# Performance work log

Hardware: AMD Instinct MI355X
Metric: run time of the kernel (lower is better)

## Reference

```python
import jax, jax.numpy as jnp
import numpy as np

B, D, H, W = 2, 32, 192, 192
N_SIGMA = 3
K = 8  # max instance id; ids are 1..K, 0 = background
FG_W = 1.0
W_INST, W_VAR, W_SEED = 1.0, 10.0, 1.0


def _make_xyzm():
    # channel 0 = x (varies along W), 1 = y (along H), 2 = z (along D); pixel_{x,y,z}=1
    xm = jnp.broadcast_to(jnp.linspace(0.0, 1.0, W).reshape(1, 1, W), (D, H, W))
    ym = jnp.broadcast_to(jnp.linspace(0.0, 1.0, H).reshape(1, H, 1), (D, H, W))
    zm = jnp.broadcast_to(jnp.linspace(0.0, 1.0, D).reshape(D, 1, 1), (D, H, W))
    return jnp.stack([xm, ym, zm], 0)  # (3, D, H, W)


def setup_inputs() -> dict:
    key = jax.random.key(0)
    k1, k2, k3, k4 = jax.random.split(key, 4)
    prediction = jax.random.normal(k1, (B, 3 + N_SIGMA + 1, D, H, W), jnp.float32)
    instances = jax.random.randint(k2, (B, D, H, W), 0, K + 1, jnp.int32)
    labels = jax.random.randint(k3, (B, D, H, W), 0, 2, jnp.int32)
    center_images = jax.random.uniform(k4, (B, D, H, W)) < 5e-4  # sparse center flags
    return {"prediction": prediction, "xyzm": _make_xyzm(),
            "instances": instances, "labels": labels, "center_images": center_images}


def _lovasz_hinge_flat(logits, labels):
    # logits, labels: (N,) flat; labels in {0,1} float
    signs = 2.0 * labels - 1.0
    errors = 1.0 - logits * signs
    order = jnp.argsort(-errors)          # descending errors
    errors_s = errors[order]
    gt_s = labels[order]
    gts = gt_s.sum()
    inter = gts - jnp.cumsum(gt_s)
    union = gts + jnp.cumsum(1.0 - gt_s)
    jacc = 1.0 - inter / union
    grad = jnp.concatenate([jacc[:1], jacc[1:] - jacc[:-1]])
    return jnp.dot(jax.nn.relu(errors_s), jax.lax.stop_gradient(grad))


def _forward(prediction, xyzm, instances, labels, center_images):
    def per_batch(pred, inst, lab, cim):
        emb = jnp.tanh(pred[0:3]) + xyzm                      # (3,D,H,W)
        sigma = pred[3:3 + N_SIGMA]                           # (ns,D,H,W)
        seed = jax.nn.sigmoid(pred[3 + N_SIGMA])              # (D,H,W)
        ids = jnp.arange(1, K + 1)
        masks = (inst[None] == ids[:, None, None, None]).astype(pred.dtype)  # (K,D,H,W)
        counts = masks.sum(axis=(1, 2, 3))                    # (K,)
        valid = counts > 0
        safe = jnp.maximum(counts, 1.0)
        # center: single flagged center voxel if exactly one, else masked mean of coords
        mean_center = jnp.einsum('kdhw,cdhw->kc', masks, xyzm) / safe[:, None]
        cmask = masks * cim[None].astype(pred.dtype)
        cm_cnt = cmask.sum(axis=(1, 2, 3))
        cm_center = jnp.einsum('kdhw,cdhw->kc', cmask, xyzm)
        center = jnp.where((cm_cnt == 1.0)[:, None], cm_center, mean_center)  # (K,3)
        # sigma stats per instance; var term vs detached mean, expanded form
        m_sig = jnp.einsum('kdhw,cdhw->kc', masks, sigma)
        m_sig2 = jnp.einsum('kdhw,cdhw->kc', masks, sigma * sigma)
        s_mean = m_sig / safe[:, None]                        # (K,ns)
        s_sg = jax.lax.stop_gradient(s_mean)
        var_sum = m_sig2 - 2.0 * s_sg * m_sig + s_sg * s_sg * counts[:, None]
        var_k = var_sum.sum(1) / (N_SIGMA * safe)
        s_exp = jnp.exp(10.0 * s_mean)                        # (K,ns)
        # sum_c s_c*(emb_c-center_c)^2, expanded to avoid a (K,3,D,H,W) temp
        d2 = (jnp.einsum('kc,cdhw->kdhw', s_exp, emb * emb)
              - 2.0 * jnp.einsum('kc,cdhw->kdhw', s_exp * center, emb)
              + (s_exp * center * center).sum(1)[:, None, None, None])
        dist = jnp.exp(-d2)                                   # (K,D,H,W)
        inst_k = jax.vmap(_lovasz_hinge_flat)(
            (2.0 * dist - 1.0).reshape(K, -1), masks.reshape(K, -1))
        obj = jnp.maximum(valid.sum(), 1).astype(pred.dtype)
        instance_loss = jnp.where(valid, inst_k, 0.0).sum() / obj
        var_loss = jnp.where(valid, var_k, 0.0).sum() / obj
        bg = (lab == 0).astype(pred.dtype)
        seed_loss = (bg * seed * seed).sum()
        seed_loss = seed_loss + FG_W * (masks * (seed[None] - jax.lax.stop_gradient(dist)) ** 2).sum()
        seed_loss = seed_loss / (D * H * W)
        return W_INST * instance_loss + W_VAR * var_loss + W_SEED * seed_loss

    losses = jax.vmap(per_batch)(prediction, instances, labels, center_images)
    return losses.mean()


def reference(prediction, xyzm, instances, labels, center_images):
    return _forward(prediction, xyzm, instances, labels, center_images)
```

## Files before the change

kernel.cpp:

```cpp
#include <hip/hip_runtime.h>
#include <stdint.h>

typedef unsigned long long u64;
typedef unsigned int u32;

#define BN 2
#define DD 32
#define HH 192
#define WW 192
#define NV (DD*HH*WW)
#define KK 8
#define NSL_S 576
#define VPB_S 2048
#define NSL_H 288
#define VPB_H 4096
#define NB 256
#define BOFF 1808
#define SCALE 4294967296.0f
#define L2E 1.44269504f

__device__ __forceinline__ u64 fx(float v){ return (u64)(long long)llrintf(v*SCALE); }
__device__ __forceinline__ float unfx(u64 v){ return (float)((double)(long long)v*(1.0/4294967296.0)); }
__device__ __forceinline__ float rcp_f(float x){ return __builtin_amdgcn_rcpf(x); }
__device__ __forceinline__ float exp2_f(float x){ return __builtin_amdgcn_exp2f(x); }
__device__ __forceinline__ float tanh_f(float x){ return 1.f - 2.f*rcp_f(1.f + exp2_f(x*(2.f*L2E))); }
__device__ __forceinline__ float sigm_f(float x){ return rcp_f(1.f + exp2_f(-x*L2E)); }
__device__ __forceinline__ float rfl(float x){ return __uint_as_float(__builtin_amdgcn_readfirstlane((int)__float_as_uint(x))); }

__global__ void k_detect(const u32* __restrict__ w, int nwords, u32* flags){
    u32 fF=0,fB=0,fO=0,f1=0;
    for (int i = blockIdx.x*blockDim.x + threadIdx.x; i < nwords; i += gridDim.x*blockDim.x){
        u32 x = w[i];
        if (x == 0x3F800000u) fF = 1;
        else if (x > 1u) fB = 1;
        else if (x == 1u){ f1 = 1; if (i & 1) fO = 1; }
    }
    if (fF) atomicOr(&flags[0], 1u);
    if (fB) atomicOr(&flags[1], 1u);
    if (fO) atomicOr(&flags[2], 1u);
    if (f1) atomicOr(&flags[3], 1u);
}

__global__ __launch_bounds__(512, 8) void k_stats(
        const float* __restrict__ pred,
        const int* __restrict__ inst, const int* __restrict__ lab,
        const void* __restrict__ cim, const u32* __restrict__ flags,
        u64* __restrict__ ssh, u64* __restrict__ bgsh){
    int sx = blockIdx.x, b = blockIdx.y;
    __shared__ u64 bins[8][4][KK][9];
    __shared__ u64 cmb[8][KK][4];
    __shared__ u64 bgsum;
    for (int i = threadIdx.x; i < 8*4*KK*9; i += 512) ((u64*)bins)[i] = 0ull;
    for (int i = threadIdx.x; i < 8*KK*4; i += 512) ((u64*)cmb)[i] = 0ull;
    if (threadIdx.x == 0) bgsum = 0ull;
    __syncthreads();
    int mode = flags[0] ? 2 : (flags[1] ? 1 : (flags[2] ? 0 : (flags[3] ? 3 : 0)));
    const float* pb = pred + (size_t)b*7*NV;
    const int* ib = inst + (size_t)b*NV;
    const int* lb = lab + (size_t)b*NV;
    int wv = threadIdx.x >> 6, lp = threadIdx.x & 3;
    int g = sx*VPB_S + threadIdx.x*4;

    float4 s0v = *(const float4*)&pb[3*(size_t)NV + g];
    float4 s1v = *(const float4*)&pb[4*(size_t)NV + g];
    float4 s2v = *(const float4*)&pb[5*(size_t)NV + g];
    float4 s6v = *(const float4*)&pb[6*(size_t)NV + g];
    int4 iv4 = *(const int4*)&ib[g];
    int4 lb4 = *(const int4*)&lb[g];
    int iy = g / WW;
    int ix = g - iy*WW;
    int iz = iy / HH; iy -= iz*HH;
    u64 fdx = fx(1.f/(WW-1));
    u64 fxm = fx(ix*(1.f/(WW-1)));
    u64 fym = fx(iy*(1.f/(HH-1)));
    u64 fzm = fx(iz*(1.f/(DD-1)));
    u32 cv4 = 0;
    size_t gi = (size_t)b*NV + g;
    if (mode == 0){
        int4 c = *(const int4*)&((const int*)cim)[gi];
        cv4 = (c.x?1u:0u)|(c.y?2u:0u)|(c.z?4u:0u)|(c.w?8u:0u);
    } else if (mode == 1){
        u32 c = *(const u32*)&((const unsigned char*)cim)[gi];
        cv4 = ((c&0xFFu)?1u:0u)|((c&0xFF00u)?2u:0u)|((c&0xFF0000u)?4u:0u)|((c&0xFF000000u)?8u:0u);
    } else if (mode == 2){
        float4 c = *(const float4*)&((const float*)cim)[gi];
        cv4 = (c.x!=0.f?1u:0u)|(c.y!=0.f?2u:0u)|(c.z!=0.f?4u:0u)|(c.w!=0.f?8u:0u);
    } else {
        int4 c0 = *(const int4*)&((const int*)cim)[2*gi];
        int4 c1 = *(const int4*)&((const int*)cim)[2*gi + 4];
        cv4 = (c0.x?1u:0u)|(c0.z?2u:0u)|(c1.x?4u:0u)|(c1.z?8u:0u);
    }
    float s0a[4] = {s0v.x,s0v.y,s0v.z,s0v.w};
    float s1a[4] = {s1v.x,s1v.y,s1v.z,s1v.w};
    float s2a[4] = {s2v.x,s2v.y,s2v.z,s2v.w};
    float s6a[4] = {s6v.x,s6v.y,s6v.z,s6v.w};
    int iva[4] = {iv4.x,iv4.y,iv4.z,iv4.w};
    int lba[4] = {lb4.x,lb4.y,lb4.z,lb4.w};
    float bgacc = 0.f;
    #pragma unroll
    for (int j = 0; j < 4; j++){
        float seed = sigm_f(s6a[j]);
        if (lba[j] == 0) bgacc += seed*seed;
        int iv = iva[j];
        if (iv >= 1 && iv <= KK){
            u64* bn = &bins[wv][lp][iv-1][0];
            u32 cv = (cv4 >> j) & 1u;
            atomicAdd(&bn[0], (1ull << 32) | (u64)cv);
            atomicAdd(&bn[1], fxm + (u64)j*fdx);
            atomicAdd(&bn[2], fym);
            atomicAdd(&bn[3], fzm);
            atomicAdd(&bn[4], fx(s0a[j]));
            atomicAdd(&bn[5], fx(s1a[j]));
            atomicAdd(&bn[6], fx(s2a[j]));
            atomicAdd(&bn[7], fx(s0a[j]*s0a[j] + s1a[j]*s1a[j] + s2a[j]*s2a[j]));
            if (cv){
                u64* cb = &cmb[wv][iv-1][0];
                atomicAdd(&cb[0], fxm + (u64)j*fdx);
                atomicAdd(&cb[1], fym);
                atomicAdd(&cb[2], fzm);
            }
        }
    }
    #pragma unroll
    for (int off = 32; off > 0; off >>= 1) bgacc += __shfl_down(bgacc, off);
    if ((threadIdx.x & 63) == 0 && bgacc != 0.f) atomicAdd(&bgsum, fx(bgacc));
    __syncthreads();
    if (threadIdx.x == 0 && bgsum) atomicAdd(&bgsh[(size_t)b*8 + (sx&7)], bgsum);
    for (int i = threadIdx.x; i < KK*8; i += 512){
        int k = i >> 3, s = i & 7;
        u64 acc = 0ull;
        #pragma unroll
        for (int r = 0; r < 32; r++) acc += bins[r>>2][r&3][k][s];
        if (acc) atomicAdd(&ssh[((size_t)((sx&3)*BN + b)*KK + k)*12 + s], acc);
    }
    for (int i = threadIdx.x; i < KK*3; i += 512){
        int k = i / 3, s = i - k*3;
        u64 acc = 0ull;
        #pragma unroll
        for (int w = 0; w < 8; w++) acc += cmb[w][k][s];
        if (acc) atomicAdd(&ssh[((size_t)((sx&3)*BN + b)*KK + k)*12 + 8 + s], acc);
    }
}

__global__ void k_derive(const u64* __restrict__ ssh, float* __restrict__ derived,
                         float* __restrict__ var_part){
    int t = threadIdx.x;
    __shared__ float s_val[16], s_vrk[16], s_obj[2];
    if (t < 16){
        int bb = t >> 3, kq = t & 7;
        u64 st[12];
        #pragma unroll
        for (int s = 0; s < 12; s++){
            u64 a = 0ull;
            #pragma unroll
            for (int sh = 0; sh < 4; sh++)
                a += ssh[((size_t)(sh*BN + bb)*KK + kq)*12 + s];
            st[s] = a;
        }
        float cnt = (float)(long long)(st[0] >> 32);
        float cmc = (float)(u32)(st[0] & 0xFFFFFFFFull);
        float sxs = unfx(st[1]), sys = unfx(st[2]), szs = unfx(st[3]);
        float g0 = unfx(st[4]), g1 = unfx(st[5]), g2 = unfx(st[6]);
        float h = unfx(st[7]);
        float cmx = unfx(st[8]), cmy = unfx(st[9]), cmz = unfx(st[10]);
        float valid = cnt > 0.f ? 1.f : 0.f;
        float safe = fmaxf(cnt, 1.f);
        float c0 = (cmc == 1.f) ? cmx : sxs/safe;
        float c1 = (cmc == 1.f) ? cmy : sys/safe;
        float c2 = (cmc == 1.f) ? cmz : szs/safe;
        float sm0 = g0/safe, sm1 = g1/safe, sm2 = g2/safe;
        float vs = h - 2.f*(sm0*g0 + sm1*g1 + sm2*g2)
                 + (sm0*sm0 + sm1*sm1 + sm2*sm2)*cnt;
        s_vrk[t] = vs / (3.f*safe);
        s_val[t] = valid;
        float* dd = &derived[(size_t)t*8];
        dd[0] = expf(10.f*sm0); dd[1] = expf(10.f*sm1); dd[2] = expf(10.f*sm2);
        dd[3] = c0; dd[4] = c1; dd[5] = c2; dd[6] = cnt;
    }
    __syncthreads();
    if (t < 2){
        float obj = 0.f, vp = 0.f;
        #pragma unroll
        for (int kq = 0; kq < 8; kq++){
            obj += s_val[t*8 + kq];
            vp += s_val[t*8 + kq]*s_vrk[t*8 + kq];
        }
        obj = fmaxf(obj, 1.f);
        var_part[t] = vp / obj;
        s_obj[t] = obj;
    }
    __syncthreads();
    if (t < 16) derived[(size_t)t*8 + 7] = s_val[t]/s_obj[t >> 3];
}

__global__ __launch_bounds__(512, 4) void k_hist(
        const float* __restrict__ pred,
        const int* __restrict__ inst, const float* __restrict__ derived,
        u32* __restrict__ hs, u64* __restrict__ bgsh){
    __shared__ u32 lh[KK*2*NB];
    __shared__ u64 fgfx;
    int sx = blockIdx.x, b = blockIdx.y;
    if (threadIdx.x == 0) fgfx = 0ull;
    for (int i = threadIdx.x; i < KK*2*NB; i += 512) lh[i] = 0u;
    float ax[KK], ay[KK], az[KK], cx[KK], cy[KK], cz[KK];
    const float* db = derived + (size_t)b*KK*8;
    #pragma unroll
    for (int k = 0; k < KK; k++){
        ax[k]=rfl(db[k*8+0])*L2E; ay[k]=rfl(db[k*8+1])*L2E; az[k]=rfl(db[k*8+2])*L2E;
        cx[k]=rfl(db[k*8+3]); cy[k]=rfl(db[k*8+4]); cz[k]=rfl(db[k*8+5]);
    }
    __syncthreads();
    const float* pb = pred + (size_t)b*7*NV;
    const int* ib = inst + (size_t)b*NV;
    int g = sx*VPB_H + threadIdx.x*8;
    const float4* q0 = (const float4*)&pb[g];
    const float4* q1 = (const float4*)&pb[(size_t)NV + g];
    const float4* q2 = (const float4*)&pb[2*(size_t)NV + g];
    const float4* q6 = (const float4*)&pb[6*(size_t)NV + g];
    float4 a0 = q0[0], b0 = q0[1];
    float4 a1 = q1[0], b1 = q1[1];
    float4 a2 = q2[0], b2 = q2[1];
    float4 a6 = q6[0], b6 = q6[1];
    const int4* qi = (const int4*)&ib[g];
    int4 i0 = qi[0], i1 = qi[1];
    int iy = g / WW;
    int ix = g - iy*WW;
    int iz = iy / HH; iy -= iz*HH;
    float xm = ix*(1.f/(WW-1)), ym = iy*(1.f/(HH-1)), zm = iz*(1.f/(DD-1));
    float p0a[8] = {a0.x,a0.y,a0.z,a0.w,b0.x,b0.y,b0.z,b0.w};
    float p1a[8] = {a1.x,a1.y,a1.z,a1.w,b1.x,b1.y,b1.z,b1.w};
    float p2a[8] = {a2.x,a2.y,a2.z,a2.w,b2.x,b2.y,b2.z,b2.w};
    float p6a[8] = {a6.x,a6.y,a6.z,a6.w,b6.x,b6.y,b6.z,b6.w};
    int iva[8] = {i0.x,i0.y,i0.z,i0.w,i1.x,i1.y,i1.z,i1.w};
    float e0[8], e1[8], e2[8], sd[8];
    #pragma unroll
    for (int j = 0; j < 8; j++){
        e0[j] = tanh_f(p0a[j]) + xm + j*(1.f/(WW-1));
        e1[j] = tanh_f(p1a[j]) + ym;
        e2[j] = tanh_f(p2a[j]) + zm;
        sd[j] = sigm_f(p6a[j]);
    }
    float fgacc = 0.f;
    #pragma unroll
    for (int k = 0; k < KK; k++){
        #pragma unroll
        for (int j = 0; j < 8; j++){
            float d0 = e0[j] - cx[k], d1 = e1[j] - cy[k], dz = e2[j] - cz[k];
            float d2 = ax[k]*d0*d0;
            d2 = fmaf(ay[k]*d1, d1, d2);
            d2 = fmaf(az[k]*dz, dz, d2);
            float dist = exp2_f(-d2);
            if (iva[j] == k + 1){
                float e = fmaf(-2.f, dist, 2.f);
                int bu = (int)(__float_as_uint(e) >> 19) - BOFF;
                bu = bu < 0 ? 0 : (bu > NB-1 ? NB-1 : bu);
                atomicAdd(&lh[k*512 + bu], 1u);
                fgacc += (sd[j] - dist)*(sd[j] - dist);
            } else {
                int bu = (int)(__float_as_uint(dist) >> 19) - (BOFF - 16);
                bu = bu < 0 ? 0 : (bu > NB-1 ? NB-1 : bu);
                atomicAdd(&lh[k*512 + NB + bu], 1u);
            }
        }
    }
    #pragma unroll
    for (int off = 32; off > 0; off >>= 1) fgacc += __shfl_down(fgacc, off);
    if ((threadIdx.x & 63) == 0 && fgacc != 0.f) atomicAdd(&fgfx, fx(fgacc));
    __syncthreads();
    if (threadIdx.x == 0 && fgfx) atomicAdd(&bgsh[(size_t)(2+b)*8 + (sx&7)], fgfx);
    u32* out = hs + ((size_t)b*NSL_H + sx)*(KK*NB);
    for (int i = threadIdx.x; i < KK*NB; i += 512){
        int k = i >> 8, bu = i & 255;
        out[i] = (lh[k*512 + bu] << 16) | lh[k*512 + NB + bu];
    }
}

__global__ __launch_bounds__(1024) void k_lovasz(
        const u32* __restrict__ hs, const float* __restrict__ derived,
        float* __restrict__ lov, const float* __restrict__ var_part,
        const u64* __restrict__ bgsh, u32* __restrict__ counter,
        float* __restrict__ out){
    int bk = blockIdx.x, b = bk >> 3, k = bk & 7;
    int t = threadIdx.x;
    float gts = derived[(size_t)bk*8 + 6];
    float lv = 0.f;
    __shared__ u64 part[4][NB];
    __shared__ u64 wsum[4];
    __shared__ float racc[NB];
    if (gts >= 0.5f){
        int bu = (NB - 1) - (t & 255);
        int sg = t >> 8;
        u32 np = 0, nn = 0;
        const u32* base = hs + (size_t)b*NSL_H*(KK*NB) + k*NB + bu;
        for (int s = sg; s < NSL_H; s += 4){
            u32 h = base[(size_t)s*(KK*NB)];
            np += h >> 16; nn += h & 0xFFFFu;
        }
        part[sg][t & 255] = ((u64)np << 32) | nn;
        __syncthreads();
        u64 pack = 0ull, inc = 0ull;
        if (t < NB){
            pack = part[0][t] + part[1][t] + part[2][t] + part[3][t];
            int lane = t & 63;
            inc = pack;
            #pragma unroll
            for (int off = 1; off < 64; off <<= 1){
                u64 n = __shfl_up(inc, off);
                if (lane >= off) inc += n;
            }
            if (lane == 63) wsum[t >> 6] = inc;
        }
        __syncthreads();
        if (t < 4){
            u64 x = wsum[t];
            #pragma unroll
            for (int off = 1; off < 4; off <<= 1){
                u64 n = __shfl_up(x, off);
                if (t >= off) x += n;
            }
            wsum[t] = x;
        }
        __syncthreads();
        float acc = 0.f;
        if (t < NB){
            int wid = t >> 6;
            u64 excl = inc - pack + (wid ? wsum[wid - 1] : 0ull);
            u32 np2 = (u32)(pack >> 32), nn2 = (u32)pack;
            if (np2 | nn2){
                int bu2 = (NB - 1) - t;
                float Pe = (float)(u32)(excl >> 32), Qe = (float)(u32)excl;
                float Pi = Pe + (float)np2, Qi = Qe + (float)nn2;
                float je = 1.f - (gts - Pe)/(gts + Qe);
                float ji = 1.f - (gts - Pi)/(gts + Qi);
                u32 bits = ((u32)(bu2 + BOFF) << 19) | (1u << 18);
                if (bits > 0x40000000u) bits = 0x40000000u;
                acc = __uint_as_float(bits) * (ji - je);
            }
            racc[t] = acc;
        }
        __syncthreads();
        for (int off = 128; off > 0; off >>= 1){
            if (t < off) racc[t] += racc[t + off];
            __syncthreads();
        }
        lv = derived[(size_t)bk*8 + 7] * racc[0];
    }
    if (t == 0){
        __hip_atomic_store(&lov[bk], lv, __ATOMIC_RELEASE, __HIP_MEMORY_SCOPE_AGENT);
        u32 ticket = __hip_atomic_fetch_add(counter, 1u, __ATOMIC_ACQ_REL, __HIP_MEMORY_SCOPE_AGENT);
        if (ticket == 15u){
            float tot = 0.f;
            for (int i = 0; i < 16; i++)
                tot += __hip_atomic_load(&lov[i], __ATOMIC_ACQUIRE, __HIP_MEMORY_SCOPE_AGENT);
            for (int b2 = 0; b2 < BN; b2++){
                float bg = 0.f, fg = 0.f;
                for (int sh = 0; sh < 8; sh++){
                    bg += unfx(bgsh[(size_t)b2*8 + sh]);
                    fg += unfx(bgsh[(size_t)(2+b2)*8 + sh]);
                }
                tot += 10.f*var_part[b2] + (bg + fg)*(1.f/(float)NV);
            }
            out[0] = tot * 0.5f;
        }
    }
}

extern "C" void kernel_launch(void* const* d_in, const int* in_sizes, int n_in,
                              void* d_out, int out_size, void* d_ws, size_t ws_size,
                              hipStream_t stream){
    const float* pred = (const float*)d_in[0];
    const int*   inst = (const int*)d_in[2];
    const int*   lab  = (const int*)d_in[3];
    const void*  cim  = d_in[4];

    char* ws = (char*)d_ws;
    size_t off = 0;
    u32* hs = (u32*)(ws + off);        off += (size_t)BN*NSL_H*KK*NB*4;
    size_t small0 = off;
    u64* ssh = (u64*)(ws + off);       off += (size_t)4*BN*KK*12*8;
    u64* bgsh = (u64*)(ws + off);      off += (size_t)4*8*8;
    float* derived = (float*)(ws + off); off += (size_t)BN*KK*8*4;
    float* lov = (float*)(ws + off);   off += 16*4;
    float* var_part = (float*)(ws + off); off += 2*4;
    u32* flags = (u32*)(ws + off);     off += 4*4;
    u32* counter = (u32*)(ws + off);   off += 4;

    (void)hipMemsetAsync(ws + small0, 0, off - small0, stream);
    k_detect<<<dim3(256), dim3(256), 0, stream>>>((const u32*)cim, BN*NV/4, flags);
    k_stats<<<dim3(NSL_S, BN), dim3(512), 0, stream>>>(pred, inst, lab, cim, flags, ssh, bgsh);
    k_derive<<<1, 64, 0, stream>>>(ssh, derived, var_part);
    k_hist<<<dim3(NSL_H, BN), dim3(512), 0, stream>>>(pred, inst, derived, hs, bgsh);
    k_lovasz<<<16, 1024, 0, stream>>>(hs, derived, lov, var_part, bgsh, counter, (float*)d_out);
}
```

Before: 76.46 us.

## Fold derive kernel into hist/lovasz and shrink stats bins to 32-bit

Removes the single-block k_derive launch by having k_hist and k_lovasz each recompute the per-instance derived values directly from the reduced stats buffer. Shared-memory bins in k_stats switch from 64-bit to 32-bit atomics, using integer voxel coordinates and 12-bit fixed-point sigma sums, with z packed into the count word. This saves one kernel launch and halves the LDS atomic width, at the cost of lower precision for the sigma sums, a risk of 32-bit overflow in the packed fields, and some duplicated per-block setup work.

After: 81.65 us. 1.07x slower.

```diff
diff --git a/kernel.cpp b/kernel.cpp
--- a/kernel.cpp
+++ b/kernel.cpp
@@ -16,16 +16,41 @@
 #define VPB_H 4096
 #define NB 256
 #define BOFF 1808
-#define SCALE 4294967296.0f
 #define L2E 1.44269504f
-
-__device__ __forceinline__ u64 fx(float v){ return (u64)(long long)llrintf(v*SCALE); }
+#define SSLOT 11
+
+__device__ __forceinline__ u64 fx(float v){ return (u64)(long long)llrintf(v*4294967296.0f); }
 __device__ __forceinline__ float unfx(u64 v){ return (float)((double)(long long)v*(1.0/4294967296.0)); }
+__device__ __forceinline__ u32 fx12(float v){ return (u32)(int)llrintf(v*4096.0f); }
+__device__ __forceinline__ float unfx12(u64 v){ return (float)((double)(long long)v*(1.0/4096.0)); }
 __device__ __forceinline__ float rcp_f(float x){ return __builtin_amdgcn_rcpf(x); }
 __device__ __forceinline__ float exp2_f(float x){ return __builtin_amdgcn_exp2f(x); }
 __device__ __forceinline__ float tanh_f(float x){ return 1.f - 2.f*rcp_f(1.f + exp2_f(x*(2.f*L2E))); }
 __device__ __forceinline__ float sigm_f(float x){ return rcp_f(1.f + exp2_f(-x*L2E)); }
 __device__ __forceinline__ float rfl(float x){ return __uint_as_float(__builtin_amdgcn_readfirstlane((int)__float_as_uint(x))); }
+
+struct Cell { float cnt, cmc, mx, my, mz, g0, g1, g2, h, cmx, cmy, cmz; };
+__device__ __forceinline__ Cell load_cell(const u64* __restrict__ ssh, int bb, int kq){
+    u64 st[SSLOT];
+    #pragma unroll
+    for (int s = 0; s < SSLOT; s++){
+        u64 a = 0ull;
+        #pragma unroll
+        for (int sh = 0; sh < 4; sh++)
+            a += ssh[((size_t)(sh*BN + bb)*KK + kq)*SSLOT + s];
+        st[s] = a;
+    }
+    Cell c;
+    c.cnt = (float)(long long)(st[0] >> 32);
+    c.cmc = (float)(u32)st[0];
+    c.mx = (float)(long long)st[1] * (1.f/(WW-1));
+    c.my = (float)(long long)st[2] * (1.f/(HH-1));
+    c.mz = (float)(long long)st[3] * (1.f/(DD-1));
+    c.g0 = unfx12(st[4]); c.g1 = unfx12(st[5]); c.g2 = unfx12(st[6]);
+    c.h  = unfx12(st[7]);
+    c.cmx = unfx(st[8]); c.cmy = unfx(st[9]); c.cmz = unfx(st[10]);
+    return c;
+}
 
 __global__ void k_detect(const u32* __restrict__ w, int nwords, u32* flags){
     u32 fF=0,fB=0,fO=0,f1=0;
@@ -47,10 +72,10 @@
         const void* __restrict__ cim, const u32* __restrict__ flags,
         u64* __restrict__ ssh, u64* __restrict__ bgsh){
     int sx = blockIdx.x, b = blockIdx.y;
-    __shared__ u64 bins[8][4][KK][9];
+    __shared__ u32 bins32[8][4][KK][7];
     __shared__ u64 cmb[8][KK][4];
     __shared__ u64 bgsum;
-    for (int i = threadIdx.x; i < 8*4*KK*9; i += 512) ((u64*)bins)[i] = 0ull;
+    for (int i = threadIdx.x; i < 8*4*KK*7; i += 512) ((u32*)bins32)[i] = 0u;
     for (int i = threadIdx.x; i < 8*KK*4; i += 512) ((u64*)cmb)[i] = 0ull;
     if (threadIdx.x == 0) bgsum = 0ull;
     __syncthreads();
@@ -70,8 +95,8 @@
     int iy = g / WW;
     int ix = g - iy*WW;
     int iz = iy / HH; iy -= iz*HH;
+    u64 fxm = fx(ix*(1.f/(WW-1)));
     u64 fdx = fx(1.f/(WW-1));
-    u64 fxm = fx(ix*(1.f/(WW-1)));
     u64 fym = fx(iy*(1.f/(HH-1)));
     u64 fzm = fx(iz*(1.f/(DD-1)));
     u32 cv4 = 0;
@@ -103,16 +128,15 @@
         if (lba[j] == 0) bgacc += seed*seed;
         int iv = iva[j];
         if (iv >= 1 && iv <= KK){
-            u64* bn = &bins[wv][lp][iv-1][0];
+            u32* bn = &bins32[wv][lp][iv-1][0];
             u32 cv = (cv4 >> j) & 1u;
-            atomicAdd(&bn[0], (1ull << 32) | (u64)cv);
-            atomicAdd(&bn[1], fxm + (u64)j*fdx);
-            atomicAdd(&bn[2], fym);
-            atomicAdd(&bn[3], fzm);
-            atomicAdd(&bn[4], fx(s0a[j]));
-            atomicAdd(&bn[5], fx(s1a[j]));
-            atomicAdd(&bn[6], fx(s2a[j]));
-            atomicAdd(&bn[7], fx(s0a[j]*s0a[j] + s1a[j]*s1a[j] + s2a[j]*s2a[j]));
+            atomicAdd(&bn[0], (1u << 20) | ((u32)iz << 4) | cv);
+            atomicAdd(&bn[1], (u32)(ix + j));
+            atomicAdd(&bn[2], (u32)iy);
+            atomicAdd(&bn[3], fx12(s0a[j]));
+            atomicAdd(&bn[4], fx12(s1a[j]));
+            atomicAdd(&bn[5], fx12(s2a[j]));
+            atomicAdd(&bn[6], fx12(s0a[j]*s0a[j] + s1a[j]*s1a[j] + s2a[j]*s2a[j]));
             if (cv){
                 u64* cb = &cmb[wv][iv-1][0];
                 atomicAdd(&cb[0], fxm + (u64)j*fdx);
@@ -126,90 +150,64 @@
     if ((threadIdx.x & 63) == 0 && bgacc != 0.f) atomicAdd(&bgsum, fx(bgacc));
     __syncthreads();
     if (threadIdx.x == 0 && bgsum) atomicAdd(&bgsh[(size_t)b*8 + (sx&7)], bgsum);
-    for (int i = threadIdx.x; i < KK*8; i += 512){
-        int k = i >> 3, s = i & 7;
-        u64 acc = 0ull;
+    int t = threadIdx.x;
+    u64* cell0 = &ssh[((size_t)((sx&3)*BN + b))*KK*SSLOT];
+    if (t < KK*7){
+        int k = t / 7, s = t - k*7;
+        u32 acc = 0u;
         #pragma unroll
-        for (int r = 0; r < 32; r++) acc += bins[r>>2][r&3][k][s];
-        if (acc) atomicAdd(&ssh[((size_t)((sx&3)*BN + b)*KK + k)*12 + s], acc);
-    }
-    for (int i = threadIdx.x; i < KK*3; i += 512){
-        int k = i / 3, s = i - k*3;
+        for (int r = 0; r < 32; r++) acc += bins32[r>>2][r&3][k][s];
+        u64* cell = cell0 + (size_t)k*SSLOT;
+        if (s == 0){
+            if (acc){
+                u64 cnt = acc >> 20, siz = (acc >> 4) & 0xFFFFu, cm = acc & 15u;
+                atomicAdd(&cell[0], (cnt << 32) | cm);
+                if (siz) atomicAdd(&cell[3], siz);
+            }
+        } else if (s < 3){
+            if (acc) atomicAdd(&cell[s], (u64)acc);
+        } else {
+            if (acc) atomicAdd(&cell[s + 1], (u64)(long long)(int)acc);
+        }
+    }
+    if (t < KK*3){
+        int k = t / 3, s = t - k*3;
         u64 acc = 0ull;
         #pragma unroll
         for (int w = 0; w < 8; w++) acc += cmb[w][k][s];
-        if (acc) atomicAdd(&ssh[((size_t)((sx&3)*BN + b)*KK + k)*12 + 8 + s], acc);
-    }
-}
-
-__global__ void k_derive(const u64* __restrict__ ssh, float* __restrict__ derived,
-                         float* __restrict__ var_part){
-    int t = threadIdx.x;
-    __shared__ float s_val[16], s_vrk[16], s_obj[2];
-    if (t < 16){
-        int bb = t >> 3, kq = t & 7;
-        u64 st[12];
-        #pragma unroll
-        for (int s = 0; s < 12; s++){
-            u64 a = 0ull;
-            #pragma unroll
-            for (int sh = 0; sh < 4; sh++)
-                a += ssh[((size_t)(sh*BN + bb)*KK + kq)*12 + s];
-            st[s] = a;
-        }
-        float cnt = (float)(long long)(st[0] >> 32);
-        float cmc = (float)(u32)(st[0] & 0xFFFFFFFFull);
-        float sxs = unfx(st[1]), sys = unfx(st[2]), szs = unfx(st[3]);
-        float g0 = unfx(st[4]), g1 = unfx(st[5]), g2 = unfx(st[6]);
-        float h = unfx(st[7]);
-        float cmx = unfx(st[8]), cmy = unfx(st[9]), cmz = unfx(st[10]);
-        float valid = cnt > 0.f ? 1.f : 0.f;
-        float safe = fmaxf(cnt, 1.f);
-        float c0 = (cmc == 1.f) ? cmx : sxs/safe;
-        float c1 = (cmc == 1.f) ? cmy : sys/safe;
-        float c2 = (cmc == 1.f) ? cmz : szs/safe;
-        float sm0 = g0/safe, sm1 = g1/safe, sm2 = g2/safe;
-        float vs = h - 2.f*(sm0*g0 + sm1*g1 + sm2*g2)
-                 + (sm0*sm0 + sm1*sm1 + sm2*sm2)*cnt;
-        s_vrk[t] = vs / (3.f*safe);
-        s_val[t] = valid;
-        float* dd = &derived[(size_t)t*8];
-        dd[0] = expf(10.f*sm0); dd[1] = expf(10.f*sm1); dd[2] = expf(10.f*sm2);
-        dd[3] = c0; dd[4] = c1; dd[5] = c2; dd[6] = cnt;
-    }
-    __syncthreads();
-    if (t < 2){
-        float obj = 0.f, vp = 0.f;
-        #pragma unroll
-        for (int kq = 0; kq < 8; kq++){
-            obj += s_val[t*8 + kq];
-            vp += s_val[t*8 + kq]*s_vrk[t*8 + kq];
-        }
-        obj = fmaxf(obj, 1.f);
-        var_part[t] = vp / obj;
-        s_obj[t] = obj;
-    }
-    __syncthreads();
-    if (t < 16) derived[(size_t)t*8 + 7] = s_val[t]/s_obj[t >> 3];
+        if (acc) atomicAdd(&cell0[(size_t)k*SSLOT + 8 + s], acc);
+    }
 }
 
 __global__ __launch_bounds__(512, 4) void k_hist(
-        const float* __restrict__ pred,
-        const int* __restrict__ inst, const float* __restrict__ derived,
-        u32* __restrict__ hs, u64* __restrict__ bgsh){
+        const u64* __restrict__ ssh, const float* __restrict__ pred,
+        const int* __restrict__ inst, u32* __restrict__ hs, u64* __restrict__ bgsh){
     __shared__ u32 lh[KK*2*NB];
     __shared__ u64 fgfx;
+    __shared__ float dv[KK*6];
     int sx = blockIdx.x, b = blockIdx.y;
     if (threadIdx.x == 0) fgfx = 0ull;
     for (int i = threadIdx.x; i < KK*2*NB; i += 512) lh[i] = 0u;
+    if (threadIdx.x < KK){
+        int kq = threadIdx.x;
+        Cell c = load_cell(ssh, b, kq);
+        float safe = fmaxf(c.cnt, 1.f);
+        float isafe = 1.f/safe;
+        float c0 = (c.cmc == 1.f) ? c.cmx : c.mx*isafe;
+        float c1 = (c.cmc == 1.f) ? c.cmy : c.my*isafe;
+        float c2 = (c.cmc == 1.f) ? c.cmz : c.mz*isafe;
+        dv[kq*6+0] = expf(10.f*c.g0*isafe)*L2E;
+        dv[kq*6+1] = expf(10.f*c.g1*isafe)*L2E;
+        dv[kq*6+2] = expf(10.f*c.g2*isafe)*L2E;
+        dv[kq*6+3] = c0; dv[kq*6+4] = c1; dv[kq*6+5] = c2;
+    }
+    __syncthreads();
     float ax[KK], ay[KK], az[KK], cx[KK], cy[KK], cz[KK];
-    const float* db = derived + (size_t)b*KK*8;
     #pragma unroll
     for (int k = 0; k < KK; k++){
-        ax[k]=rfl(db[k*8+0])*L2E; ay[k]=rfl(db[k*8+1])*L2E; az[k]=rfl(db[k*8+2])*L2E;
-        cx[k]=rfl(db[k*8+3]); cy[k]=rfl(db[k*8+4]); cz[k]=rfl(db[k*8+5]);
-    }
-    __syncthreads();
+        ax[k]=rfl(dv[k*6+0]); ay[k]=rfl(dv[k*6+1]); az[k]=rfl(dv[k*6+2]);
+        cx[k]=rfl(dv[k*6+3]); cy[k]=rfl(dv[k*6+4]); cz[k]=rfl(dv[k*6+5]);
+    }
     const float* pb = pred + (size_t)b*7*NV;
     const int* ib = inst + (size_t)b*NV;
     int g = sx*VPB_H + threadIdx.x*8;
@@ -276,13 +274,28 @@
 }
 
 __global__ __launch_bounds__(1024) void k_lovasz(
-        const u32* __restrict__ hs, const float* __restrict__ derived,
-        float* __restrict__ lov, const float* __restrict__ var_part,
-        const u64* __restrict__ bgsh, u32* __restrict__ counter,
-        float* __restrict__ out){
+        const u32* __restrict__ hs, const u64* __restrict__ ssh,
+        float* __restrict__ lov, const u64* __restrict__ bgsh,
+        u32* __restrict__ counter, float* __restrict__ out){
     int bk = blockIdx.x, b = bk >> 3, k = bk & 7;
     int t = threadIdx.x;
-    float gts = derived[(size_t)bk*8 + 6];
+    __shared__ float s_cnt[16], s_vrk[16], s_val[16];
+    if (t < 16){
+        Cell c = load_cell(ssh, t >> 3, t & 7);
+        float safe = fmaxf(c.cnt, 1.f);
+        float isafe = 1.f/safe;
+        float sm0 = c.g0*isafe, sm1 = c.g1*isafe, sm2 = c.g2*isafe;
+        float vs = c.h - 2.f*(sm0*c.g0 + sm1*c.g1 + sm2*c.g2)
+                 + (sm0*sm0 + sm1*sm1 + sm2*sm2)*c.cnt;
+        s_vrk[t] = vs*isafe*(1.f/3.f);
+        s_val[t] = c.cnt > 0.f ? 1.f : 0.f;
+        s_cnt[t] = c.cnt;
+    }
+    __syncthreads();
+    float gts = s_cnt[bk];
+    float obj = fmaxf(s_val[b*8+0]+s_val[b*8+1]+s_val[b*8+2]+s_val[b*8+3]
+                     +s_val[b*8+4]+s_val[b*8+5]+s_val[b*8+6]+s_val[b*8+7], 1.f);
+    float coef = s_val[bk]/obj;
     float lv = 0.f;
     __shared__ u64 part[4][NB];
     __shared__ u64 wsum[4];
@@ -343,7 +356,7 @@
             if (t < off) racc[t] += racc[t + off];
             __syncthreads();
         }
-        lv = derived[(size_t)bk*8 + 7] * racc[0];
+        lv = coef * racc[0];
     }
     if (t == 0){
         __hip_atomic_store(&lov[bk], lv, __ATOMIC_RELEASE, __HIP_MEMORY_SCOPE_AGENT);
@@ -353,12 +366,16 @@
             for (int i = 0; i < 16; i++)
                 tot += __hip_atomic_load(&lov[i], __ATOMIC_ACQUIRE, __HIP_MEMORY_SCOPE_AGENT);
             for (int b2 = 0; b2 < BN; b2++){
+                float objb = fmaxf(s_val[b2*8+0]+s_val[b2*8+1]+s_val[b2*8+2]+s_val[b2*8+3]
+                                  +s_val[b2*8+4]+s_val[b2*8+5]+s_val[b2*8+6]+s_val[b2*8+7], 1.f);
+                float vp = 0.f;
+                for (int kq = 0; kq < 8; kq++) vp += s_val[b2*8+kq]*s_vrk[b2*8+kq];
                 float bg = 0.f, fg = 0.f;
                 for (int sh = 0; sh < 8; sh++){
                     bg += unfx(bgsh[(size_t)b2*8 + sh]);
                     fg += unfx(bgsh[(size_t)(2+b2)*8 + sh]);
                 }
-                tot += 10.f*var_part[b2] + (bg + fg)*(1.f/(float)NV);
+                tot += 10.f*vp/objb + (bg + fg)*(1.f/(float)NV);
             }
             out[0] = tot * 0.5f;
         }
@@ -377,18 +394,15 @@
     size_t off = 0;
     u32* hs = (u32*)(ws + off);        off += (size_t)BN*NSL_H*KK*NB*4;
     size_t small0 = off;
-    u64* ssh = (u64*)(ws + off);       off += (size_t)4*BN*KK*12*8;
+    u64* ssh = (u64*)(ws + off);       off += (size_t)4*BN*KK*SSLOT*8;
     u64* bgsh = (u64*)(ws + off);      off += (size_t)4*8*8;
-    float* derived = (float*)(ws + off); off += (size_t)BN*KK*8*4;
     float* lov = (float*)(ws + off);   off += 16*4;
-    float* var_part = (float*)(ws + off); off += 2*4;
     u32* flags = (u32*)(ws + off);     off += 4*4;
     u32* counter = (u32*)(ws + off);   off += 4;
 
     (void)hipMemsetAsync(ws + small0, 0, off - small0, stream);
     k_detect<<<dim3(256), dim3(256), 0, stream>>>((const u32*)cim, BN*NV/4, flags);
     k_stats<<<dim3(NSL_S, BN), dim3(512), 0, stream>>>(pred, inst, lab, cim, flags, ssh, bgsh);
-    k_derive<<<1, 64, 0, stream>>>(ssh, derived, var_part);
-    k_hist<<<dim3(NSL_H, BN), dim3(512), 0, stream>>>(pred, inst, derived, hs, bgsh);
-    k_lovasz<<<16, 1024, 0, stream>>>(hs, derived, lov, var_part, bgsh, counter, (float*)d_out);
-}
+    k_hist<<<dim3(NSL_H, BN), dim3(512), 0, stream>>>(ssh, pred, inst, hs, bgsh);
+    k_lovasz<<<16, 1024, 0, stream>>>(hs, ssh, lov, bgsh, counter, (float*)d_out);
+}
```

## Pack per-instance stats into fewer bit-packed atomics and move bg seed term to hist

Applied to the files above, without the earlier changes.

The stats kernel now packs count, x/y index sums and center flags into one 64-bit atomic, and quantized sigma sums and squared norms into two more, cutting shared atomics per voxel from eight to three. It processes eight voxels per thread with half the blocks. The background seed loss and label loads move into the histogram kernel, which already reads the seed channel, so the stats kernel no longer reads label or seed data. The cost is reduced precision from fixed-point quantization and clamping of sigma values, plus a risk of bit-field overflow in the packed sums.

After: 78.05 us. 2.1% more time.

```diff
diff --git a/kernel.cpp b/kernel.cpp
--- a/kernel.cpp
+++ b/kernel.cpp
@@ -10,16 +10,14 @@
 #define WW 192
 #define NV (DD*HH*WW)
 #define KK 8
-#define NSL_S 576
-#define VPB_S 2048
-#define NSL_H 288
-#define VPB_H 4096
+#define NSL 288
+#define VPB 4096
 #define NB 256
 #define BOFF 1808
-#define SCALE 4294967296.0f
 #define L2E 1.44269504f
-
-__device__ __forceinline__ u64 fx(float v){ return (u64)(long long)llrintf(v*SCALE); }
+#define SSLOT 11
+
+__device__ __forceinline__ u64 fx(float v){ return (u64)(long long)llrintf(v*4294967296.0f); }
 __device__ __forceinline__ float unfx(u64 v){ return (float)((double)(long long)v*(1.0/4294967296.0)); }
 __device__ __forceinline__ float rcp_f(float x){ return __builtin_amdgcn_rcpf(x); }
 __device__ __forceinline__ float exp2_f(float x){ return __builtin_amdgcn_exp2f(x); }
@@ -43,76 +41,76 @@
 
 __global__ __launch_bounds__(512, 8) void k_stats(
         const float* __restrict__ pred,
-        const int* __restrict__ inst, const int* __restrict__ lab,
+        const int* __restrict__ inst,
         const void* __restrict__ cim, const u32* __restrict__ flags,
         u64* __restrict__ ssh, u64* __restrict__ bgsh){
     int sx = blockIdx.x, b = blockIdx.y;
-    __shared__ u64 bins[8][4][KK][9];
+    __shared__ u64 bins[8][4][25];
     __shared__ u64 cmb[8][KK][4];
-    __shared__ u64 bgsum;
-    for (int i = threadIdx.x; i < 8*4*KK*9; i += 512) ((u64*)bins)[i] = 0ull;
+    for (int i = threadIdx.x; i < 8*4*25; i += 512) ((u64*)bins)[i] = 0ull;
     for (int i = threadIdx.x; i < 8*KK*4; i += 512) ((u64*)cmb)[i] = 0ull;
-    if (threadIdx.x == 0) bgsum = 0ull;
     __syncthreads();
     int mode = flags[0] ? 2 : (flags[1] ? 1 : (flags[2] ? 0 : (flags[3] ? 3 : 0)));
     const float* pb = pred + (size_t)b*7*NV;
     const int* ib = inst + (size_t)b*NV;
-    const int* lb = lab + (size_t)b*NV;
     int wv = threadIdx.x >> 6, lp = threadIdx.x & 3;
-    int g = sx*VPB_S + threadIdx.x*4;
-
-    float4 s0v = *(const float4*)&pb[3*(size_t)NV + g];
-    float4 s1v = *(const float4*)&pb[4*(size_t)NV + g];
-    float4 s2v = *(const float4*)&pb[5*(size_t)NV + g];
-    float4 s6v = *(const float4*)&pb[6*(size_t)NV + g];
-    int4 iv4 = *(const int4*)&ib[g];
-    int4 lb4 = *(const int4*)&lb[g];
+    int g = sx*VPB + threadIdx.x*8;
+
+    const float4* q0p = (const float4*)&pb[3*(size_t)NV + g];
+    const float4* q1p = (const float4*)&pb[4*(size_t)NV + g];
+    const float4* q2p = (const float4*)&pb[5*(size_t)NV + g];
+    float4 sa0 = q0p[0], sb0 = q0p[1];
+    float4 sa1 = q1p[0], sb1 = q1p[1];
+    float4 sa2 = q2p[0], sb2 = q2p[1];
+    const int4* qi = (const int4*)&ib[g];
+    int4 i0 = qi[0], i1 = qi[1];
     int iy = g / WW;
     int ix = g - iy*WW;
     int iz = iy / HH; iy -= iz*HH;
+    u64 fxm = fx(ix*(1.f/(WW-1)));
     u64 fdx = fx(1.f/(WW-1));
-    u64 fxm = fx(ix*(1.f/(WW-1)));
     u64 fym = fx(iy*(1.f/(HH-1)));
     u64 fzm = fx(iz*(1.f/(DD-1)));
-    u32 cv4 = 0;
+    u32 cv8 = 0;
     size_t gi = (size_t)b*NV + g;
     if (mode == 0){
-        int4 c = *(const int4*)&((const int*)cim)[gi];
-        cv4 = (c.x?1u:0u)|(c.y?2u:0u)|(c.z?4u:0u)|(c.w?8u:0u);
+        int4 c0 = ((const int4*)&((const int*)cim)[gi])[0];
+        int4 c1 = ((const int4*)&((const int*)cim)[gi])[1];
+        cv8 = (c0.x?1u:0u)|(c0.y?2u:0u)|(c0.z?4u:0u)|(c0.w?8u:0u)
+            | (c1.x?16u:0u)|(c1.y?32u:0u)|(c1.z?64u:0u)|(c1.w?128u:0u);
     } else if (mode == 1){
-        u32 c = *(const u32*)&((const unsigned char*)cim)[gi];
-        cv4 = ((c&0xFFu)?1u:0u)|((c&0xFF00u)?2u:0u)|((c&0xFF0000u)?4u:0u)|((c&0xFF000000u)?8u:0u);
+        u64 c = *(const u64*)&((const unsigned char*)cim)[gi];
+        #pragma unroll
+        for (int j = 0; j < 8; j++) if ((c >> (8*j)) & 0xFFull) cv8 |= 1u << j;
     } else if (mode == 2){
-        float4 c = *(const float4*)&((const float*)cim)[gi];
-        cv4 = (c.x!=0.f?1u:0u)|(c.y!=0.f?2u:0u)|(c.z!=0.f?4u:0u)|(c.w!=0.f?8u:0u);
+        float4 c0 = ((const float4*)&((const float*)cim)[gi])[0];
+        float4 c1 = ((const float4*)&((const float*)cim)[gi])[1];
+        cv8 = (c0.x!=0.f?1u:0u)|(c0.y!=0.f?2u:0u)|(c0.z!=0.f?4u:0u)|(c0.w!=0.f?8u:0u)
+            | (c1.x!=0.f?16u:0u)|(c1.y!=0.f?32u:0u)|(c1.z!=0.f?64u:0u)|(c1.w!=0.f?128u:0u);
     } else {
-        int4 c0 = *(const int4*)&((const int*)cim)[2*gi];
-        int4 c1 = *(const int4*)&((const int*)cim)[2*gi + 4];
-        cv4 = (c0.x?1u:0u)|(c0.z?2u:0u)|(c1.x?4u:0u)|(c1.z?8u:0u);
-    }
-    float s0a[4] = {s0v.x,s0v.y,s0v.z,s0v.w};
-    float s1a[4] = {s1v.x,s1v.y,s1v.z,s1v.w};
-    float s2a[4] = {s2v.x,s2v.y,s2v.z,s2v.w};
-    float s6a[4] = {s6v.x,s6v.y,s6v.z,s6v.w};
-    int iva[4] = {iv4.x,iv4.y,iv4.z,iv4.w};
-    int lba[4] = {lb4.x,lb4.y,lb4.z,lb4.w};
-    float bgacc = 0.f;
+        const int4* cc = (const int4*)&((const int*)cim)[2*gi];
+        int4 c0 = cc[0], c1 = cc[1], c2 = cc[2], c3 = cc[3];
+        cv8 = (c0.x?1u:0u)|(c0.z?2u:0u)|(c1.x?4u:0u)|(c1.z?8u:0u)
+            | (c2.x?16u:0u)|(c2.z?32u:0u)|(c3.x?64u:0u)|(c3.z?128u:0u);
+    }
+    float s0a[8] = {sa0.x,sa0.y,sa0.z,sa0.w,sb0.x,sb0.y,sb0.z,sb0.w};
+    float s1a[8] = {sa1.x,sa1.y,sa1.z,sa1.w,sb1.x,sb1.y,sb1.z,sb1.w};
+    float s2a[8] = {sa2.x,sa2.y,sa2.z,sa2.w,sb2.x,sb2.y,sb2.z,sb2.w};
+    int iva[8] = {i0.x,i0.y,i0.z,i0.w,i1.x,i1.y,i1.z,i1.w};
     #pragma unroll
-    for (int j = 0; j < 4; j++){
-        float seed = sigm_f(s6a[j]);
-        if (lba[j] == 0) bgacc += seed*seed;
+    for (int j = 0; j < 8; j++){
         int iv = iva[j];
         if (iv >= 1 && iv <= KK){
-            u64* bn = &bins[wv][lp][iv-1][0];
-            u32 cv = (cv4 >> j) & 1u;
-            atomicAdd(&bn[0], (1ull << 32) | (u64)cv);
-            atomicAdd(&bn[1], fxm + (u64)j*fdx);
-            atomicAdd(&bn[2], fym);
-            atomicAdd(&bn[3], fzm);
-            atomicAdd(&bn[4], fx(s0a[j]));
-            atomicAdd(&bn[5], fx(s1a[j]));
-            atomicAdd(&bn[6], fx(s2a[j]));
-            atomicAdd(&bn[7], fx(s0a[j]*s0a[j] + s1a[j]*s1a[j] + s2a[j]*s2a[j]));
+            u64* bn = &bins[wv][lp][(iv-1)*3];
+            u32 cv = (cv8 >> j) & 1u;
+            u32 q0 = (u32)llrintf((s0a[j] + 16.f)*4096.f);
+            u32 q1 = (u32)llrintf((s1a[j] + 16.f)*4096.f);
+            u32 q2 = (u32)llrintf((s2a[j] + 16.f)*4096.f);
+            float s2t = s0a[j]*s0a[j] + s1a[j]*s1a[j] + s2a[j]*s2a[j];
+            u32 r = (u32)llrintf(fminf(s2t, 512.f)*2048.f);
+            atomicAdd(&bn[0], (1ull << 44) | ((u64)(u32)(ix + j) << 24) | ((u64)(u32)iy << 4) | cv);
+            atomicAdd(&bn[1], ((u64)q0 << 32) | q1);
+            atomicAdd(&bn[2], ((u64)q2 << 32) | r);
             if (cv){
                 u64* cb = &cmb[wv][iv-1][0];
                 atomicAdd(&cb[0], fxm + (u64)j*fdx);
@@ -121,24 +119,44 @@
             }
         }
     }
-    #pragma unroll
-    for (int off = 32; off > 0; off >>= 1) bgacc += __shfl_down(bgacc, off);
-    if ((threadIdx.x & 63) == 0 && bgacc != 0.f) atomicAdd(&bgsum, fx(bgacc));
-    __syncthreads();
-    if (threadIdx.x == 0 && bgsum) atomicAdd(&bgsh[(size_t)b*8 + (sx&7)], bgsum);
-    for (int i = threadIdx.x; i < KK*8; i += 512){
-        int k = i >> 3, s = i & 7;
+    __syncthreads();
+    int t = threadIdx.x;
+    u64* cell0 = &ssh[((size_t)((sx&3)*BN + b))*KK*SSLOT];
+    if (t < KK){
+        int k = t;
+        u64 sA = 0ull, sB = 0ull, sC = 0ull;
+        #pragma unroll
+        for (int r2 = 0; r2 < 32; r2++){
+            const u64* bn = &bins[r2>>2][r2&3][k*3];
+            sA += bn[0]; sB += bn[1]; sC += bn[2];
+        }
+        u64 cnt = sA >> 44;
+        if (cnt){
+            u64 six = (sA >> 24) & 0xFFFFFull;
+            u64 siy = (sA >> 4) & 0xFFFFFull;
+            u64 cm  = sA & 0xFull;
+            long long bias = (long long)(cnt * 65536ull);
+            long long g0 = (long long)(sB >> 32) - bias;
+            long long g1 = (long long)(sB & 0xFFFFFFFFull) - bias;
+            long long g2 = (long long)(sC >> 32) - bias;
+            u64 h = sC & 0xFFFFFFFFull;
+            u64* cell = cell0 + (size_t)k*SSLOT;
+            atomicAdd(&cell[0], (cnt << 32) | cm);
+            atomicAdd(&cell[1], six);
+            atomicAdd(&cell[2], siy);
+            atomicAdd(&cell[3], cnt*(u64)iz);
+            atomicAdd(&cell[4], (u64)g0);
+            atomicAdd(&cell[5], (u64)g1);
+            atomicAdd(&cell[6], (u64)g2);
+            atomicAdd(&cell[7], h);
+        }
+    }
+    if (t < KK*3){
+        int k = t / 3, s = t - k*3;
         u64 acc = 0ull;
         #pragma unroll
-        for (int r = 0; r < 32; r++) acc += bins[r>>2][r&3][k][s];
-        if (acc) atomicAdd(&ssh[((size_t)((sx&3)*BN + b)*KK + k)*12 + s], acc);
-    }
-    for (int i = threadIdx.x; i < KK*3; i += 512){
-        int k = i / 3, s = i - k*3;
-        u64 acc = 0ull;
-        #pragma unroll
         for (int w = 0; w < 8; w++) acc += cmb[w][k][s];
-        if (acc) atomicAdd(&ssh[((size_t)((sx&3)*BN + b)*KK + k)*12 + 8 + s], acc);
+        if (acc) atomicAdd(&cell0[(size_t)k*SSLOT + 8 + s], acc);
     }
 }
 
@@ -148,33 +166,38 @@
     __shared__ float s_val[16], s_vrk[16], s_obj[2];
     if (t < 16){
         int bb = t >> 3, kq = t & 7;
-        u64 st[12];
-        #pragma unroll
-        for (int s = 0; s < 12; s++){
+        u64 st[SSLOT];
+        #pragma unroll
+        for (int s = 0; s < SSLOT; s++){
             u64 a = 0ull;
             #pragma unroll
             for (int sh = 0; sh < 4; sh++)
-                a += ssh[((size_t)(sh*BN + bb)*KK + kq)*12 + s];
+                a += ssh[((size_t)(sh*BN + bb)*KK + kq)*SSLOT + s];
             st[s] = a;
         }
         float cnt = (float)(long long)(st[0] >> 32);
-        float cmc = (float)(u32)(st[0] & 0xFFFFFFFFull);
-        float sxs = unfx(st[1]), sys = unfx(st[2]), szs = unfx(st[3]);
-        float g0 = unfx(st[4]), g1 = unfx(st[5]), g2 = unfx(st[6]);
-        float h = unfx(st[7]);
+        float cmc = (float)(u32)st[0];
+        float mx = (float)(long long)st[1] * (1.f/(WW-1));
+        float my = (float)(long long)st[2] * (1.f/(HH-1));
+        float mz = (float)(long long)st[3] * (1.f/(DD-1));
+        float g0 = (float)((double)(long long)st[4] * (1.0/4096.0));
+        float g1 = (float)((double)(long long)st[5] * (1.0/4096.0));
+        float g2 = (float)((double)(long long)st[6] * (1.0/4096.0));
+        float h  = (float)((double)(long long)st[7] * (1.0/2048.0));
         float cmx = unfx(st[8]), cmy = unfx(st[9]), cmz = unfx(st[10]);
         float valid = cnt > 0.f ? 1.f : 0.f;
         float safe = fmaxf(cnt, 1.f);
-        float c0 = (cmc == 1.f) ? cmx : sxs/safe;
-        float c1 = (cmc == 1.f) ? cmy : sys/safe;
-        float c2 = (cmc == 1.f) ? cmz : szs/safe;
-        float sm0 = g0/safe, sm1 = g1/safe, sm2 = g2/safe;
+        float isafe = 1.f/safe;
+        float c0 = (cmc == 1.f) ? cmx : mx*isafe;
+        float c1 = (cmc == 1.f) ? cmy : my*isafe;
+        float c2 = (cmc == 1.f) ? cmz : mz*isafe;
+        float sm0 = g0*isafe, sm1 = g1*isafe, sm2 = g2*isafe;
         float vs = h - 2.f*(sm0*g0 + sm1*g1 + sm2*g2)
                  + (sm0*sm0 + sm1*sm1 + sm2*sm2)*cnt;
-        s_vrk[t] = vs / (3.f*safe);
+        s_vrk[t] = vs*isafe*(1.f/3.f);
         s_val[t] = valid;
         float* dd = &derived[(size_t)t*8];
-        dd[0] = expf(10.f*sm0); dd[1] = expf(10.f*sm1); dd[2] = expf(10.f*sm2);
+        dd[0] = expf(10.f*sm0)*L2E; dd[1] = expf(10.f*sm1)*L2E; dd[2] = expf(10.f*sm2)*L2E;
         dd[3] = c0; dd[4] = c1; dd[5] = c2; dd[6] = cnt;
     }
     __syncthreads();
@@ -195,24 +218,26 @@
 
 __global__ __launch_bounds__(512, 4) void k_hist(
         const float* __restrict__ pred,
-        const int* __restrict__ inst, const float* __restrict__ derived,
+        const int* __restrict__ inst, const int* __restrict__ lab,
+        const float* __restrict__ derived,
         u32* __restrict__ hs, u64* __restrict__ bgsh){
     __shared__ u32 lh[KK*2*NB];
-    __shared__ u64 fgfx;
+    __shared__ u64 fgfx, bgfx;
     int sx = blockIdx.x, b = blockIdx.y;
-    if (threadIdx.x == 0) fgfx = 0ull;
+    if (threadIdx.x == 0){ fgfx = 0ull; bgfx = 0ull; }
     for (int i = threadIdx.x; i < KK*2*NB; i += 512) lh[i] = 0u;
     float ax[KK], ay[KK], az[KK], cx[KK], cy[KK], cz[KK];
     const float* db = derived + (size_t)b*KK*8;
     #pragma unroll
     for (int k = 0; k < KK; k++){
-        ax[k]=rfl(db[k*8+0])*L2E; ay[k]=rfl(db[k*8+1])*L2E; az[k]=rfl(db[k*8+2])*L2E;
+        ax[k]=rfl(db[k*8+0]); ay[k]=rfl(db[k*8+1]); az[k]=rfl(db[k*8+2]);
         cx[k]=rfl(db[k*8+3]); cy[k]=rfl(db[k*8+4]); cz[k]=rfl(db[k*8+5]);
     }
     __syncthreads();
     const float* pb = pred + (size_t)b*7*NV;
     const int* ib = inst + (size_t)b*NV;
-    int g = sx*VPB_H + threadIdx.x*8;
+    const int* lb = lab + (size_t)b*NV;
+    int g = sx*VPB + threadIdx.x*8;
     const float4* q0 = (const float4*)&pb[g];
     const float4* q1 = (const float4*)&pb[(size_t)NV + g];
     const float4* q2 = (const float4*)&pb[2*(size_t)NV + g];
@@ -223,6 +248,8 @@
     float4 a6 = q6[0], b6 = q6[1];
     const int4* qi = (const int4*)&ib[g];
     int4 i0 = qi[0], i1 = qi[1];
+    const int4* ql = (const int4*)&lb[g];
+    int4 l0 = ql[0], l1 = ql[1];
     int iy = g / WW;
     int ix = g - iy*WW;
     int iz = iy / HH; iy -= iz*HH;
@@ -232,13 +259,16 @@
     float p2a[8] = {a2.x,a2.y,a2.z,a2.w,b2.x,b2.y,b2.z,b2.w};
     float p6a[8] = {a6.x,a6.y,a6.z,a6.w,b6.x,b6.y,b6.z,b6.w};
     int iva[8] = {i0.x,i0.y,i0.z,i0.w,i1.x,i1.y,i1.z,i1.w};
+    int lba[8] = {l0.x,l0.y,l0.z,l0.w,l1.x,l1.y,l1.z,l1.w};
     float e0[8], e1[8], e2[8], sd[8];
+    float bgacc = 0.f;
     #pragma unroll
     for (int j = 0; j < 8; j++){
         e0[j] = tanh_f(p0a[j]) + xm + j*(1.f/(WW-1));
         e1[j] = tanh_f(p1a[j]) + ym;
         e2[j] = tanh_f(p2a[j]) + zm;
         sd[j] = sigm_f(p6a[j]);
+        if (lba[j] == 0) bgacc += sd[j]*sd[j];
     }
     float fgacc = 0.f;
     #pragma unroll
@@ -264,11 +294,20 @@
         }
     }
     #pragma unroll
-    for (int off = 32; off > 0; off >>= 1) fgacc += __shfl_down(fgacc, off);
-    if ((threadIdx.x & 63) == 0 && fgacc != 0.f) atomicAdd(&fgfx, fx(fgacc));
-    __syncthreads();
-    if (threadIdx.x == 0 && fgfx) atomicAdd(&bgsh[(size_t)(2+b)*8 + (sx&7)], fgfx);
-    u32* out = hs + ((size_t)b*NSL_H + sx)*(KK*NB);
+    for (int off = 32; off > 0; off >>= 1){
+        fgacc += __shfl_down(fgacc, off);
+        bgacc += __shfl_down(bgacc, off);
+    }
+    if ((threadIdx.x & 63) == 0){
+        if (fgacc != 0.f) atomicAdd(&fgfx, fx(fgacc));
+        if (bgacc != 0.f) atomicAdd(&bgfx, fx(bgacc));
+    }
+    __syncthreads();
+    if (threadIdx.x == 0){
+        if (bgfx) atomicAdd(&bgsh[(size_t)b*8 + (sx&7)], bgfx);
+        if (fgfx) atomicAdd(&bgsh[(size_t)(2+b)*8 + (sx&7)], fgfx);
+    }
+    u32* out = hs + ((size_t)b*NSL + sx)*(KK*NB);
     for (int i = threadIdx.x; i < KK*NB; i += 512){
         int k = i >> 8, bu = i & 255;
         out[i] = (lh[k*512 + bu] << 16) | lh[k*512 + NB + bu];
@@ -291,8 +330,8 @@
         int bu = (NB - 1) - (t & 255);
         int sg = t >> 8;
         u32 np = 0, nn = 0;
-        const u32* base = hs + (size_t)b*NSL_H*(KK*NB) + k*NB + bu;
-        for (int s = sg; s < NSL_H; s += 4){
+        const u32* base = hs + (size_t)b*NSL*(KK*NB) + k*NB + bu;
+        for (int s = sg; s < NSL; s += 4){
             u32 h = base[(size_t)s*(KK*NB)];
             np += h >> 16; nn += h & 0xFFFFu;
         }
@@ -375,9 +414,9 @@
 
     char* ws = (char*)d_ws;
     size_t off = 0;
-    u32* hs = (u32*)(ws + off);        off += (size_t)BN*NSL_H*KK*NB*4;
+    u32* hs = (u32*)(ws + off);        off += (size_t)BN*NSL*KK*NB*4;
     size_t small0 = off;
-    u64* ssh = (u64*)(ws + off);       off += (size_t)4*BN*KK*12*8;
+    u64* ssh = (u64*)(ws + off);       off += (size_t)4*BN*KK*SSLOT*8;
     u64* bgsh = (u64*)(ws + off);      off += (size_t)4*8*8;
     float* derived = (float*)(ws + off); off += (size_t)BN*KK*8*4;
     float* lov = (float*)(ws + off);   off += 16*4;
@@ -387,8 +426,8 @@
 
     (void)hipMemsetAsync(ws + small0, 0, off - small0, stream);
     k_detect<<<dim3(256), dim3(256), 0, stream>>>((const u32*)cim, BN*NV/4, flags);
-    k_stats<<<dim3(NSL_S, BN), dim3(512), 0, stream>>>(pred, inst, lab, cim, flags, ssh, bgsh);
+    k_stats<<<dim3(NSL, BN), dim3(512), 0, stream>>>(pred, inst, cim, flags, ssh, bgsh);
     k_derive<<<1, 64, 0, stream>>>(ssh, derived, var_part);
-    k_hist<<<dim3(NSL_H, BN), dim3(512), 0, stream>>>(pred, inst, derived, hs, bgsh);
+    k_hist<<<dim3(NSL, BN), dim3(512), 0, stream>>>(pred, inst, lab, derived, hs, bgsh);
     k_lovasz<<<16, 1024, 0, stream>>>(hs, derived, lov, var_part, bgsh, counter, (float*)d_out);
 }
```
